# Kernel optimization log

Measured on AMD Instinct MI355X. Metric: run time of the kernel, lower is better.

Reference implementation:

```python
import jax, jax.numpy as jnp
import numpy as np
import math

SIGMA_DATA = 0.5
SIGMA_MIN = 0.002
SIGMA_MAX = 80.0
B = 32768
STATE = 256
ACT = 64
TD = 16
E = 16
H = 256  # moe hidden = gate_dim = output_dim = hidden_dim//4
IN = STATE + ACT + TD  # 336
TOP_K = 4


def mish(x):
    return x * jnp.tanh(jax.nn.softplus(x))


def setup_inputs() -> dict:
    key = jax.random.key(0)
    ks = jax.random.split(key, 20)
    def xavier(k, shape):
        fan_in, fan_out = shape[-2], shape[-1]
        lim = math.sqrt(6.0 / (fan_in + fan_out))
        return jax.random.uniform(k, shape, jnp.float32, -lim, lim)
    inp = {
        "x": jax.random.normal(ks[0], (B, ACT), jnp.float32),
        "sigma": jax.random.uniform(ks[1], (B,), jnp.float32) * (SIGMA_MAX - SIGMA_MIN) + SIGMA_MIN,
        "state": jax.random.normal(ks[2], (B, STATE), jnp.float32),
        # time MLP: Linear(16,32), Mish, Linear(32,16)
        "tW1": xavier(ks[3], (TD, 2 * TD)), "tb1": jnp.zeros((2 * TD,), jnp.float32),
        "tW2": xavier(ks[4], (2 * TD, TD)), "tb2": jnp.zeros((TD,), jnp.float32),
        # gate: Linear(IN, H), ReLU, (dropout eval), Linear(H, E)
        "gW1": xavier(ks[5], (IN, H)), "gb1": jnp.zeros((H,), jnp.float32),
        "gW2": xavier(ks[6], (H, E)), "gb2": jnp.zeros((E,), jnp.float32),
        # 16 stacked expert MLPs: IN->H->H->H with Mish after each Linear
        "eW1": xavier(ks[7], (E, IN, H)), "eb1": jnp.zeros((E, H), jnp.float32),
        "eW2": xavier(ks[8], (E, H, H)), "eb2": jnp.zeros((E, H), jnp.float32),
        "eW3": xavier(ks[9], (E, H, H)), "eb3": jnp.zeros((E, H), jnp.float32),
        # final layer: Linear(H, ACT)
        "fW": xavier(ks[10], (H, ACT)), "fb": jnp.zeros((ACT,), jnp.float32),
    }
    return inp


def reference(x, sigma, state, tW1, tb1, tW2, tb2, gW1, gb1, gW2, gb2,
              eW1, eb1, eW2, eb2, eW3, eb3, fW, fb):
    # --- consistency-model scalings (boundary condition) ---
    c_skip = SIGMA_DATA ** 2 / ((sigma - SIGMA_MIN) ** 2 + SIGMA_DATA ** 2)
    c_out = (sigma - SIGMA_MIN) * SIGMA_DATA * jax.lax.rsqrt(sigma ** 2 + SIGMA_DATA ** 2)
    c_in = jax.lax.rsqrt(sigma ** 2 + SIGMA_DATA ** 2)
    rescaled_t = 1000.0 * 0.25 * jnp.log(sigma + 1e-44)

    x_in = c_in[:, None] * x

    # --- sinusoidal time embedding (dim=16) + time MLP ---
    half = TD // 2
    freqs = jnp.exp(jnp.arange(half, dtype=jnp.float32) * (-math.log(10000.0) / (half - 1)))
    ang = rescaled_t[:, None] * freqs[None, :]           # [B, 8]
    pe = jnp.concatenate([jnp.sin(ang), jnp.cos(ang)], axis=-1)  # [B, 16]
    t = mish(pe @ tW1 + tb1) @ tW2 + tb2                 # [B, 16]

    inp = jnp.concatenate([x_in, t, state], axis=1)      # [B, 336]

    # --- gate (eval mode: dropout off) ---
    g = jax.nn.relu(inp @ gW1 + gb1) @ gW2 + gb2         # [B, E]
    gate_scores = jax.nn.softmax(g, axis=1)
    top_k_scores, top_k_idx = jax.lax.top_k(gate_scores, TOP_K)  # [B, K]

    # --- run ALL experts densely (as the original does) ---
    h = mish(jnp.einsum('bi,eih->beh', inp, eW1) + eb1)  # [B, E, H]
    h = mish(jnp.einsum('beh,ehk->bek', h, eW2) + eb2)
    expert_out = mish(jnp.einsum('beh,eho->beo', h, eW3) + eb3)  # [B, E, H]

    # --- gather top-k, scale by normalized gate scores, combine ---
    sel = jnp.take_along_axis(expert_out, top_k_idx[:, :, None], axis=1)  # [B, K, H]
    scaled = sel * top_k_scores[:, :, None]
    scaled = scaled / (jnp.sum(top_k_scores, axis=1, keepdims=True)[:, :, None] + 1e-9)
    combined = jnp.sum(scaled, axis=1)                   # [B, H]

    # --- auxiliary loss ---
    one_hot = jax.nn.one_hot(top_k_idx, E, dtype=jnp.float32)  # [B, K, E]
    expert_load = jnp.sum(one_hot, axis=(0, 1)) / (x.shape[0] + 1e-9)
    load_balancing_loss = jnp.var(expert_load, ddof=1)   # torch .var() is unbiased
    entropy = -jnp.mean(jnp.sum(gate_scores * jnp.log(gate_scores + 1e-9), axis=1))
    aux_loss = load_balancing_loss + entropy

    model_out = combined @ fW + fb                       # [B, ACT]
    denoised = c_out[:, None] * model_out + c_skip[:, None] * x
    denoised = jnp.clip(denoised, -1.0, 1.0)             # clip_denoised=True
    return denoised, aux_loss
```

## Files before the change

kernel.cpp:

```cpp
#include <hip/hip_runtime.h>
#include <math.h>

#define BN 32768
#define INDP 352
#define HD 256
#define AD 64
#define EN 16
#define TME 32
#define STOT (BN * 4)
#define GRID_E 4112
#define CHUNK_E 514

typedef __attribute__((ext_vector_type(8))) short s8v;
typedef __attribute__((ext_vector_type(4))) float f4v;
typedef unsigned short u16;

__device__ __forceinline__ u16 f2bf(float x) {
  unsigned u = __float_as_uint(x);
  return (u16)((u + 0x7fffu + ((u >> 16) & 1u)) >> 16);
}
__device__ __forceinline__ float bf2f(u16 h) { return __uint_as_float(((unsigned)h) << 16); }
__device__ __forceinline__ float rcpf(float a) { float r; asm("v_rcp_f32 %0, %1" : "=v"(r) : "v"(a)); return r; }
__device__ __forceinline__ float mishf(float x) {
  float xc = fminf(x, 30.f);
  float u = __expf(xc);
  float w = fmaf(u, u, u + u);
  return x * w * rcpf(w + 2.f);
}
__device__ __forceinline__ f4v mfma16(s8v a, s8v b, f4v c) {
  return __builtin_amdgcn_mfma_f32_16x16x32_bf16(a, b, c, 0, 0, 0);
}
__device__ __forceinline__ void pack8(const u16* q, u16* d) {
  uint4 u;
  u.x = q[0] | ((unsigned)q[1] << 16); u.y = q[2] | ((unsigned)q[3] << 16);
  u.z = q[4] | ((unsigned)q[5] << 16); u.w = q[6] | ((unsigned)q[7] << 16);
  *(uint4*)d = u;
}

__global__ void k_init(float* __restrict__ out, int* __restrict__ counts,
                       int* __restrict__ cursor, float* __restrict__ ent) {
  int i = blockIdx.x * 256 + threadIdx.x;
  if (i < BN * AD) out[i] = 0.f;
  if (i < 16) { counts[i] = 0; cursor[i] = 0; }
  if (i == 16) *ent = 0.f;
}

__global__ void k_prep(const float* __restrict__ src, u16* __restrict__ dst,
                       int Ksrc, int Spad, int NT, int N,
                       long sStride, long dStride, int NP, int total) {
  int idx = blockIdx.x * 256 + threadIdx.x;
  if (idx >= total) return;
  int l = idx & 63;
  int t = idx >> 6;
  int nt = t % NT; t /= NT;
  int s = t % Spad; t /= Spad;
  int m = t;
  const float* sp = src + (size_t)m * sStride;
  int n = nt * 16 + (l & 15);
  int kb = s * 32 + (l >> 4) * 8;
  u16 q0[8], q1[8], q2[8];
  #pragma unroll
  for (int i = 0; i < 8; ++i) {
    int k = kb + i;
    float v = (k < Ksrc) ? sp[(size_t)k * N + n] : 0.f;
    u16 a = f2bf(v); float r1 = v - bf2f(a);
    u16 b = f2bf(r1); float r2 = r1 - bf2f(b);
    q0[i] = a; q1[i] = b; q2[i] = f2bf(r2);
  }
  u16* d = dst + (size_t)m * dStride + (size_t)((s * NT + nt) * NP) * 512 + l * 8;
  pack8(q0, d);
  pack8(q1, d + 512);
  if (NP == 3) pack8(q2, d + 1024);
}

__global__ void k_time_inp(const float* __restrict__ x, const float* __restrict__ sigma,
                           const float* __restrict__ state,
                           const float* __restrict__ tW1, const float* __restrict__ tb1,
                           const float* __restrict__ tW2, const float* __restrict__ tb2,
                           u16* __restrict__ p0, u16* __restrict__ p1, u16* __restrict__ p2) {
  const int wv = threadIdx.x >> 6;
  const int lane = threadIdx.x & 63;
  const int row = blockIdx.x * 4 + wv;
  const float sg = sigma[row];
  const float rt = 250.0f * logf(sg + 1e-44f);
  float pe = 0.f;
  if (lane < 16) {
    int j = lane & 7;
    float f = expf(-1.3157629102823121f * (float)j);
    float ang = rt * f;
    pe = (lane < 8) ? sinf(ang) : cosf(ang);
  }
  float h1;
  {
    float acc = 0.f;
    int j = lane & 31;
    #pragma unroll
    for (int i = 0; i < 16; ++i) {
      float p = __shfl(pe, i, 64);
      acc = fmaf(p, tW1[i * 32 + j], acc);
    }
    acc += tb1[j];
    float sp = log1pf(expf(acc));
    h1 = acc * tanhf(sp);
  }
  float t2;
  {
    float acc = 0.f;
    int j = lane & 15;
    #pragma unroll
    for (int i = 0; i < 32; ++i) {
      float h = __shfl(h1, i, 64);
      acc = fmaf(h, tW2[i * 16 + j], acc);
    }
    t2 = acc + tb2[j];
  }
  const float c_in = rsqrtf(sg * sg + 0.25f);
  u16* r0 = p0 + (size_t)row * INDP;
  u16* r1 = p1 + (size_t)row * INDP;
  u16* r2 = p2 + (size_t)row * INDP;
  auto wsplit = [&](int c, float v) {
    u16 a = f2bf(v); float ra = v - bf2f(a);
    u16 b = f2bf(ra); float rb = ra - bf2f(b);
    r0[c] = a; r1[c] = b; r2[c] = f2bf(rb);
  };
  wsplit(lane, c_in * x[row * 64 + lane]);
  if (lane < 16) wsplit(64 + lane, t2);
  #pragma unroll
  for (int r = 0; r < 4; ++r)
    wsplit(80 + r * 64 + lane, state[(size_t)row * 256 + r * 64 + lane]);
  if (lane < 16) { r0[336 + lane] = 0; r1[336 + lane] = 0; r2[336 + lane] = 0; }
}

__global__ __launch_bounds__(256, 3) void k_gate(
    const u16* __restrict__ p0, const u16* __restrict__ p1, const u16* __restrict__ p2,
    const u16* __restrict__ gW1b, const float* __restrict__ gb1,
    const u16* __restrict__ gW2b, const float* __restrict__ gb2,
    int* __restrict__ topk_idx, float* __restrict__ topk_w,
    int* __restrict__ counts, float* __restrict__ ent_sum) {
  __shared__ __align__(16) u16 sH0[TME * 256];
  __shared__ __align__(16) u16 sH1[TME * 256];
  __shared__ __align__(16) u16 sH2[TME * 256];
  __shared__ float sLog[TME * 16];
  __shared__ int scnt[16];
  const int tid = threadIdx.x;
  const int l = tid & 63, wn = tid >> 6;
  const int g = l >> 4, r16 = l & 15;
  const int row0 = blockIdx.x * TME;
  const int swz = (r16 & 7) << 3;
  if (tid < 16) scnt[tid] = 0;

  f4v acc[2][4];
  #pragma unroll
  for (int i = 0; i < 2; ++i)
    #pragma unroll
    for (int j = 0; j < 4; ++j) acc[i][j] = (f4v){0.f, 0.f, 0.f, 0.f};

  #pragma unroll 2
  for (int s = 0; s < 11; ++s) {
    s8v a0[2], a1[2], a2[2], b0[4], b1[4], b2[4];
    #pragma unroll
    for (int mt = 0; mt < 2; ++mt) {
      size_t off = (size_t)(row0 + mt * 16 + r16) * INDP + s * 32 + g * 8;
      a0[mt] = *(const s8v*)(p0 + off);
      a1[mt] = *(const s8v*)(p1 + off);
      a2[mt] = *(const s8v*)(p2 + off);
    }
    #pragma unroll
    for (int j = 0; j < 4; ++j) {
      const u16* pb = gW1b + (size_t)((s * 16 + wn * 4 + j) * 3) * 512 + l * 8;
      b0[j] = *(const s8v*)pb;
      b1[j] = *(const s8v*)(pb + 512);
      b2[j] = *(const s8v*)(pb + 1024);
    }
    #pragma unroll
    for (int mt = 0; mt < 2; ++mt)
      #pragma unroll
      for (int j = 0; j < 4; ++j) {
        acc[mt][j] = mfma16(a0[mt], b0[j], acc[mt][j]);
        acc[mt][j] = mfma16(a0[mt], b1[j], acc[mt][j]);
        acc[mt][j] = mfma16(a1[mt], b0[j], acc[mt][j]);
        acc[mt][j] = mfma16(a1[mt], b1[j], acc[mt][j]);
        acc[mt][j] = mfma16(a0[mt], b2[j], acc[mt][j]);
        acc[mt][j] = mfma16(a2[mt], b0[j], acc[mt][j]);
      }
  }
  #pragma unroll
  for (int mt = 0; mt < 2; ++mt)
    #pragma unroll
    for (int j = 0; j < 4; ++j) {
      float bj = gb1[wn * 64 + j * 16 + r16];
      #pragma unroll
      for (int r = 0; r < 4; ++r) {
        int row = mt * 16 + g * 4 + r;
        int col = wn * 64 + j * 16 + r16;
        float v = fmaxf(acc[mt][j][r] + bj, 0.f);
        u16 h0 = f2bf(v); float ra = v - bf2f(h0);
        u16 h1 = f2bf(ra); float rb = ra - bf2f(h1);
        int ec = col ^ ((row & 7) << 3);
        sH0[row * 256 + ec] = h0;
        sH1[row * 256 + ec] = h1;
        sH2[row * 256 + ec] = f2bf(rb);
      }
    }
  __syncthreads();

  f4v l2[2];
  l2[0] = (f4v){0.f, 0.f, 0.f, 0.f};
  l2[1] = (f4v){0.f, 0.f, 0.f, 0.f};
  #pragma unroll
  for (int s = 0; s < 8; ++s) {
    const u16* pb = gW2b + (size_t)(s * 3) * 512 + l * 8;
    s8v b0 = *(const s8v*)pb;
    s8v b1 = *(const s8v*)(pb + 512);
    s8v b2 = *(const s8v*)(pb + 1024);
    #pragma unroll
    for (int mt = 0; mt < 2; ++mt) {
      int row = mt * 16 + r16;
      int ec = (s * 32 + g * 8) ^ swz;
      s8v a0 = *(const s8v*)&sH0[row * 256 + ec];
      s8v a1 = *(const s8v*)&sH1[row * 256 + ec];
      s8v a2 = *(const s8v*)&sH2[row * 256 + ec];
      l2[mt] = mfma16(a0, b0, l2[mt]);
      l2[mt] = mfma16(a0, b1, l2[mt]);
      l2[mt] = mfma16(a1, b0, l2[mt]);
      l2[mt] = mfma16(a1, b1, l2[mt]);
      l2[mt] = mfma16(a0, b2, l2[mt]);
      l2[mt] = mfma16(a2, b0, l2[mt]);
    }
  }
  if (wn == 0) {
    #pragma unroll
    for (int mt = 0; mt < 2; ++mt)
      #pragma unroll
      for (int r = 0; r < 4; ++r)
        sLog[(mt * 16 + g * 4 + r) * 16 + r16] = l2[mt][r] + gb2[r16];
  }
  __syncthreads();

  float entc = 0.f;
  if (tid < TME) {
    const int row = row0 + tid;
    float gx[16], mx = -1e30f;
    #pragma unroll
    for (int e = 0; e < 16; ++e) { gx[e] = sLog[tid * 16 + e]; mx = fmaxf(mx, gx[e]); }
    float p[16], s = 0.f;
    #pragma unroll
    for (int e = 0; e < 16; ++e) { p[e] = expf(gx[e] - mx); s += p[e]; }
    const float inv = 1.f / s;
    #pragma unroll
    for (int e = 0; e < 16; ++e) {
      float pr = p[e] * inv;
      entc -= pr * logf(pr + 1e-9f);
    }
    int idxs[4]; float scs[4];
    unsigned used = 0;
    float wsum = 1e-9f;
    #pragma unroll
    for (int k = 0; k < 4; ++k) {
      int be = 0; float bv = -1.f;
      #pragma unroll
      for (int e = 0; e < 16; ++e) {
        float pr = p[e] * inv;
        if (!((used >> e) & 1u) && pr > bv) { bv = pr; be = e; }
      }
      used |= (1u << be);
      idxs[k] = be; scs[k] = bv;
      wsum += bv;
    }
    #pragma unroll
    for (int k = 0; k < 4; ++k) {
      topk_idx[row * 4 + k] = idxs[k];
      topk_w[row * 4 + k] = scs[k] / wsum;
      atomicAdd(&scnt[idxs[k]], 1);
    }
  }
  if (tid < 64) {
    #pragma unroll
    for (int off = 32; off > 0; off >>= 1) entc += __shfl_down(entc, off, 64);
  }
  if (tid == 0) atomicAdd(ent_sum, entc);
  __syncthreads();
  if (tid < 16 && scnt[tid] > 0) atomicAdd(&counts[tid], scnt[tid]);
}

__global__ void k_aux(const int* __restrict__ counts, const float* __restrict__ ent_sum,
                      int* __restrict__ offsets, int* __restrict__ tbk,
                      float* __restrict__ aux_out) {
  if (threadIdx.x == 0) {
    int off = 0, t = 0;
    float load[16], mean = 0.f;
    for (int e = 0; e < 16; ++e) {
      offsets[e] = off; tbk[e] = t;
      int c = counts[e];
      off += c;
      t += (c + TME - 1) / TME;
      load[e] = (float)c / (32768.0f + 1e-9f);
      mean += load[e];
    }
    offsets[16] = off; tbk[16] = t;
    mean *= (1.f / 16.f);
    float var = 0.f;
    for (int e = 0; e < 16; ++e) { float d = load[e] - mean; var += d * d; }
    var *= (1.f / 15.f);
    *aux_out = var + ent_sum[0] * (1.0f / 32768.0f);
  }
}

__global__ void k_scatter(const int* __restrict__ topk_idx, const float* __restrict__ topk_w,
                          const int* __restrict__ offsets, int* __restrict__ cursor,
                          int* __restrict__ slot_row, float* __restrict__ slot_w) {
  __shared__ int cnt[16];
  __shared__ int base[16];
  const int tid = threadIdx.x;
  if (tid < 16) cnt[tid] = 0;
  __syncthreads();
  const int row = blockIdx.x * 256 + tid;
  int e4[4]; float w4[4]; int lp[4];
  #pragma unroll
  for (int k = 0; k < 4; ++k) {
    e4[k] = topk_idx[row * 4 + k];
    w4[k] = topk_w[row * 4 + k];
    lp[k] = atomicAdd(&cnt[e4[k]], 1);
  }
  __syncthreads();
  if (tid < 16) base[tid] = atomicAdd(&cursor[tid], cnt[tid]);
  __syncthreads();
  #pragma unroll
  for (int k = 0; k < 4; ++k) {
    int s = offsets[e4[k]] + base[e4[k]] + lp[k];
    slot_row[s] = row;
    slot_w[s] = w4[k];
  }
}

__global__ __launch_bounds__(256, 4) void k_expert(
    const u16* __restrict__ inpHi, const u16* __restrict__ inpLo,
    const u16* __restrict__ eW1b, const float* __restrict__ eb1,
    const u16* __restrict__ eW2b, const float* __restrict__ eb2,
    const u16* __restrict__ eW3b, const float* __restrict__ eb3,
    const u16* __restrict__ fWb,
    const int* __restrict__ offsets, const int* __restrict__ counts,
    const int* __restrict__ tbk, const int* __restrict__ slot_row,
    const float* __restrict__ slot_w, float* __restrict__ out) {
  __shared__ __align__(16) u16 sHi[TME * 256];
  __shared__ __align__(16) u16 sLo[TME * 256];
  __shared__ int sRows[TME];
  __shared__ float sWv[TME];

  const int bid = (blockIdx.x & 7) * CHUNK_E + (blockIdx.x >> 3);
  if (bid >= tbk[16]) return;
  int e = 0;
  #pragma unroll
  for (int i = 1; i < 16; ++i)
    if (bid >= tbk[i]) e = i;
  const int tile = bid - tbk[e];
  const int cnt = counts[e];
  const int s0 = offsets[e] + tile * TME;
  const int nr = min(TME, cnt - tile * TME);
  const int tid = threadIdx.x;
  const int l = tid & 63;
  const int wn = tid >> 6;
  const int g = l >> 4, r16 = l & 15;
  const int swz = (r16 & 7) << 3;

  if (tid < TME) {
    sRows[tid] = (tid < nr) ? slot_row[s0 + tid] : slot_row[s0];
    sWv[tid] = (tid < nr) ? slot_w[s0 + tid] : 0.f;
  }
  __syncthreads();

  size_t rbase[2];
  #pragma unroll
  for (int mt = 0; mt < 2; ++mt)
    rbase[mt] = (size_t)sRows[mt * 16 + r16] * INDP;

  f4v acc[2][4];
  #pragma unroll
  for (int i = 0; i < 2; ++i)
    #pragma unroll
    for (int j = 0; j < 4; ++j) acc[i][j] = (f4v){0.f, 0.f, 0.f, 0.f};

  const u16* W1 = eW1b + (size_t)e * 180224;
  #pragma unroll 2
  for (int s = 0; s < 11; ++s) {
    s8v ah[2], al[2], bh[4], bl[4];
    #pragma unroll
    for (int mt = 0; mt < 2; ++mt) {
      size_t off = rbase[mt] + s * 32 + g * 8;
      ah[mt] = *(const s8v*)(inpHi + off);
      al[mt] = *(const s8v*)(inpLo + off);
    }
    #pragma unroll
    for (int j = 0; j < 4; ++j) {
      const u16* pb = W1 + (size_t)((s * 16 + wn * 4 + j) * 2) * 512 + l * 8;
      bh[j] = *(const s8v*)pb;
      bl[j] = *(const s8v*)(pb + 512);
    }
    #pragma unroll
    for (int mt = 0; mt < 2; ++mt)
      #pragma unroll
      for (int j = 0; j < 4; ++j) {
        acc[mt][j] = mfma16(ah[mt], bh[j], acc[mt][j]);
        acc[mt][j] = mfma16(al[mt], bh[j], acc[mt][j]);
        acc[mt][j] = mfma16(ah[mt], bl[j], acc[mt][j]);
      }
  }
  {
    const float* b1 = eb1 + e * HD;
    #pragma unroll
    for (int mt = 0; mt < 2; ++mt)
      #pragma unroll
      for (int j = 0; j < 4; ++j) {
        float bj = b1[wn * 64 + j * 16 + r16];
        #pragma unroll
        for (int r = 0; r < 4; ++r) {
          int row = mt * 16 + g * 4 + r;
          int col = wn * 64 + j * 16 + r16;
          float v = mishf(acc[mt][j][r] + bj);
          u16 h = f2bf(v);
          int ec = col ^ ((row & 7) << 3);
          sHi[row * 256 + ec] = h;
          sLo[row * 256 + ec] = f2bf(v - bf2f(h));
        }
      }
  }
  __syncthreads();

  #pragma unroll 1
  for (int L = 0; L < 2; ++L) {
    const u16* Wb = (L == 0 ? eW2b : eW3b) + (size_t)e * 131072;
    const float* bb = (L == 0 ? eb2 : eb3) + e * HD;
    f4v a2[2][4];
    #pragma unroll
    for (int i = 0; i < 2; ++i)
      #pragma unroll
      for (int j = 0; j < 4; ++j) a2[i][j] = (f4v){0.f, 0.f, 0.f, 0.f};
    #pragma unroll 2
    for (int s = 0; s < 8; ++s) {
      s8v ah[2], al[2], bh[4], bl[4];
      #pragma unroll
      for (int mt = 0; mt < 2; ++mt) {
        int row = mt * 16 + r16;
        int ec = (s * 32 + g * 8) ^ swz;
        ah[mt] = *(const s8v*)&sHi[row * 256 + ec];
        al[mt] = *(const s8v*)&sLo[row * 256 + ec];
      }
      #pragma unroll
      for (int j = 0; j < 4; ++j) {
        const u16* pb = Wb + (size_t)((s * 16 + wn * 4 + j) * 2) * 512 + l * 8;
        bh[j] = *(const s8v*)pb;
        bl[j] = *(const s8v*)(pb + 512);
      }
      #pragma unroll
      for (int mt = 0; mt < 2; ++mt)
        #pragma unroll
        for (int j = 0; j < 4; ++j) {
          a2[mt][j] = mfma16(ah[mt], bh[j], a2[mt][j]);
          a2[mt][j] = mfma16(al[mt], bh[j], a2[mt][j]);
          a2[mt][j] = mfma16(ah[mt], bl[j], a2[mt][j]);
        }
    }
    __syncthreads();
    #pragma unroll
    for (int mt = 0; mt < 2; ++mt)
      #pragma unroll
      for (int j = 0; j < 4; ++j) {
        float bj = bb[wn * 64 + j * 16 + r16];
        #pragma unroll
        for (int r = 0; r < 4; ++r) {
          int row = mt * 16 + g * 4 + r;
          int col = wn * 64 + j * 16 + r16;
          float v = mishf(a2[mt][j][r] + bj);
          u16 h = f2bf(v);
          int ec = col ^ ((row & 7) << 3);
          sHi[row * 256 + ec] = h;
          sLo[row * 256 + ec] = f2bf(v - bf2f(h));
        }
      }
    __syncthreads();
  }

  f4v a3[2];
  a3[0] = (f4v){0.f, 0.f, 0.f, 0.f};
  a3[1] = (f4v){0.f, 0.f, 0.f, 0.f};
  #pragma unroll 2
  for (int s = 0; s < 8; ++s) {
    s8v ah[2], al[2];
    #pragma unroll
    for (int mt = 0; mt < 2; ++mt) {
      int row = mt * 16 + r16;
      int ec = (s * 32 + g * 8) ^ swz;
      ah[mt] = *(const s8v*)&sHi[row * 256 + ec];
      al[mt] = *(const s8v*)&sLo[row * 256 + ec];
    }
    const u16* pb = fWb + (size_t)((s * 4 + wn) * 2) * 512 + l * 8;
    s8v bh = *(const s8v*)pb;
    s8v bl = *(const s8v*)(pb + 512);
    #pragma unroll
    for (int mt = 0; mt < 2; ++mt) {
      a3[mt] = mfma16(ah[mt], bh, a3[mt]);
      a3[mt] = mfma16(al[mt], bh, a3[mt]);
      a3[mt] = mfma16(ah[mt], bl, a3[mt]);
    }
  }
  #pragma unroll
  for (int mt = 0; mt < 2; ++mt)
    #pragma unroll
    for (int r = 0; r < 4; ++r) {
      int rl = mt * 16 + g * 4 + r;
      if (rl < nr) {
        float v = a3[mt][r] * sWv[rl];
        atomicAdd(&out[(size_t)sRows[rl] * AD + wn * 16 + r16], v);
      }
    }
}

__global__ void k_final(const float* __restrict__ x, const float* __restrict__ sigma,
                        const float* __restrict__ fb, float* __restrict__ out) {
  int i = blockIdx.x * 256 + threadIdx.x;
  if (i >= BN * AD) return;
  int row = i >> 6, c = i & 63;
  float sg = sigma[row];
  float sm = sg - 0.002f;
  float c_skip = 0.25f / (sm * sm + 0.25f);
  float c_out = sm * 0.5f * rsqrtf(sg * sg + 0.25f);
  float d = c_out * (out[i] + fb[c]) + c_skip * x[i];
  out[i] = fminf(fmaxf(d, -1.f), 1.f);
}

extern "C" void kernel_launch(void* const* d_in, const int* in_sizes, int n_in,
                              void* d_out, int out_size, void* d_ws, size_t ws_size,
                              hipStream_t stream) {
  const float* x     = (const float*)d_in[0];
  const float* sigma = (const float*)d_in[1];
  const float* state = (const float*)d_in[2];
  const float* tW1   = (const float*)d_in[3];
  const float* tb1   = (const float*)d_in[4];
  const float* tW2   = (const float*)d_in[5];
  const float* tb2   = (const float*)d_in[6];
  const float* gW1   = (const float*)d_in[7];
  const float* gb1   = (const float*)d_in[8];
  const float* gW2   = (const float*)d_in[9];
  const float* gb2   = (const float*)d_in[10];
  const float* eW1   = (const float*)d_in[11];
  const float* eb1   = (const float*)d_in[12];
  const float* eW2   = (const float*)d_in[13];
  const float* eb2   = (const float*)d_in[14];
  const float* eW3   = (const float*)d_in[15];
  const float* eb3   = (const float*)d_in[16];
  const float* fW    = (const float*)d_in[17];
  const float* fb    = (const float*)d_in[18];
  float* out = (float*)d_out;

  char* p = (char*)d_ws;
  auto alloc = [&](size_t bytes) { void* r = (void*)p; p += (bytes + 255) & ~(size_t)255; return r; };
  u16* inpHi  = (u16*)alloc((size_t)BN * INDP * 2);
  u16* inpLo  = (u16*)alloc((size_t)BN * INDP * 2);
  u16* inpMid = (u16*)alloc((size_t)BN * INDP * 2);
  u16* gW1b   = (u16*)alloc((size_t)11 * 16 * 3 * 512 * 2);
  u16* gW2b   = (u16*)alloc((size_t)8 * 3 * 512 * 2);
  u16* eW1b   = (u16*)alloc((size_t)16 * 180224 * 2);
  u16* eW2b   = (u16*)alloc((size_t)16 * 131072 * 2);
  u16* eW3b   = (u16*)alloc((size_t)16 * 131072 * 2);
  u16* fWb    = (u16*)alloc((size_t)32768 * 2);
  int*   topk_idx = (int*)alloc((size_t)BN * 4 * 4);
  float* topk_w   = (float*)alloc((size_t)BN * 4 * 4);
  int*   counts   = (int*)alloc(64);
  int*   cursor   = (int*)alloc(64);
  int*   offsets  = (int*)alloc(68);
  int*   tbk      = (int*)alloc(68);
  float* ent      = (float*)alloc(4);
  int*   slot_row = (int*)alloc((size_t)STOT * 4);
  float* slot_w   = (float*)alloc((size_t)STOT * 4);

  k_init<<<(BN * AD + 255) / 256, 256, 0, stream>>>(out, counts, cursor, ent);

  int tot;
  tot = 16 * 11 * 16 * 64;
  k_prep<<<(tot + 255) / 256, 256, 0, stream>>>(eW1, eW1b, 336, 11, 16, 256,
                                                (long)336 * 256, 180224, 2, tot);
  tot = 16 * 8 * 16 * 64;
  k_prep<<<(tot + 255) / 256, 256, 0, stream>>>(eW2, eW2b, 256, 8, 16, 256,
                                                (long)256 * 256, 131072, 2, tot);
  k_prep<<<(tot + 255) / 256, 256, 0, stream>>>(eW3, eW3b, 256, 8, 16, 256,
                                                (long)256 * 256, 131072, 2, tot);
  tot = 11 * 16 * 64;
  k_prep<<<(tot + 255) / 256, 256, 0, stream>>>(gW1, gW1b, 336, 11, 16, 256,
                                                0, 0, 3, tot);
  tot = 8 * 1 * 64;
  k_prep<<<(tot + 255) / 256, 256, 0, stream>>>(gW2, gW2b, 256, 8, 1, 16,
                                                0, 0, 3, tot);
  tot = 8 * 4 * 64;
  k_prep<<<(tot + 255) / 256, 256, 0, stream>>>(fW, fWb, 256, 8, 4, 64,
                                                0, 0, 2, tot);

  k_time_inp<<<BN / 4, 256, 0, stream>>>(x, sigma, state, tW1, tb1, tW2, tb2,
                                         inpHi, inpLo, inpMid);
  k_gate<<<BN / TME, 256, 0, stream>>>(inpHi, inpLo, inpMid, gW1b, gb1, gW2b, gb2,
                                       topk_idx, topk_w, counts, ent);
  k_aux<<<1, 64, 0, stream>>>(counts, ent, offsets, tbk, out + (size_t)BN * AD);
  k_scatter<<<BN / 256, 256, 0, stream>>>(topk_idx, topk_w, offsets, cursor, slot_row, slot_w);
  k_expert<<<GRID_E, 256, 0, stream>>>(inpHi, inpLo, eW1b, eb1, eW2b, eb2,
                                       eW3b, eb3, fWb, offsets, counts, tbk,
                                       slot_row, slot_w, out);
  k_final<<<(BN * AD + 255) / 256, 256, 0, stream>>>(x, sigma, fb, out);
}
```

Baseline: 467.1 us.

## Replace atomic combine with per-slot expert outputs; shrink gate tile; reorder MFMAs

The expert kernel now writes each slot's unweighted final-layer output to a dense buffer instead of atomically adding weighted results into the output. The final kernel gathers the four slots per row through a new reverse slot map and applies the top-k weights, so zeroing the output in the init kernel is no longer needed. The gate kernel moves to 16-row tiles with a higher occupancy hint, and the MFMA chains in the gate and expert kernels are regrouped and fully unrolled so consecutive MFMAs go to independent accumulators. This trades atomic contention and an extra output clear for a new 32 MB intermediate buffer and an extra gather read in the final pass.

```diff
diff --git a/kernel.cpp b/kernel.cpp
--- a/kernel.cpp
+++ b/kernel.cpp
@@ -7,6 +7,7 @@
 #define AD 64
 #define EN 16
 #define TME 32
+#define TMG 16
 #define STOT (BN * 4)
 #define GRID_E 4112
 #define CHUNK_E 514
@@ -37,10 +38,9 @@
   *(uint4*)d = u;
 }
 
-__global__ void k_init(float* __restrict__ out, int* __restrict__ counts,
-                       int* __restrict__ cursor, float* __restrict__ ent) {
-  int i = blockIdx.x * 256 + threadIdx.x;
-  if (i < BN * AD) out[i] = 0.f;
+__global__ void k_init(int* __restrict__ counts, int* __restrict__ cursor,
+                       float* __restrict__ ent) {
+  int i = threadIdx.x;
   if (i < 16) { counts[i] = 0; cursor[i] = 0; }
   if (i == 16) *ent = 0.f;
 }
@@ -131,39 +131,36 @@
   if (lane < 16) { r0[336 + lane] = 0; r1[336 + lane] = 0; r2[336 + lane] = 0; }
 }
 
-__global__ __launch_bounds__(256, 3) void k_gate(
+__global__ __launch_bounds__(256, 4) void k_gate(
     const u16* __restrict__ p0, const u16* __restrict__ p1, const u16* __restrict__ p2,
     const u16* __restrict__ gW1b, const float* __restrict__ gb1,
     const u16* __restrict__ gW2b, const float* __restrict__ gb2,
     int* __restrict__ topk_idx, float* __restrict__ topk_w,
     int* __restrict__ counts, float* __restrict__ ent_sum) {
-  __shared__ __align__(16) u16 sH0[TME * 256];
-  __shared__ __align__(16) u16 sH1[TME * 256];
-  __shared__ __align__(16) u16 sH2[TME * 256];
-  __shared__ float sLog[TME * 16];
+  __shared__ __align__(16) u16 sH0[TMG * 256];
+  __shared__ __align__(16) u16 sH1[TMG * 256];
+  __shared__ __align__(16) u16 sH2[TMG * 256];
+  __shared__ float sLog[TMG * 16];
   __shared__ int scnt[16];
   const int tid = threadIdx.x;
   const int l = tid & 63, wn = tid >> 6;
   const int g = l >> 4, r16 = l & 15;
-  const int row0 = blockIdx.x * TME;
+  const int row0 = blockIdx.x * TMG;
   const int swz = (r16 & 7) << 3;
   if (tid < 16) scnt[tid] = 0;
 
-  f4v acc[2][4];
-  #pragma unroll
-  for (int i = 0; i < 2; ++i)
-    #pragma unroll
-    for (int j = 0; j < 4; ++j) acc[i][j] = (f4v){0.f, 0.f, 0.f, 0.f};
-
-  #pragma unroll 2
+  f4v acc[4];
+  #pragma unroll
+  for (int j = 0; j < 4; ++j) acc[j] = (f4v){0.f, 0.f, 0.f, 0.f};
+
+  #pragma unroll
   for (int s = 0; s < 11; ++s) {
-    s8v a0[2], a1[2], a2[2], b0[4], b1[4], b2[4];
-    #pragma unroll
-    for (int mt = 0; mt < 2; ++mt) {
-      size_t off = (size_t)(row0 + mt * 16 + r16) * INDP + s * 32 + g * 8;
-      a0[mt] = *(const s8v*)(p0 + off);
-      a1[mt] = *(const s8v*)(p1 + off);
-      a2[mt] = *(const s8v*)(p2 + off);
+    s8v a0, a1, a2, b0[4], b1[4], b2[4];
+    {
+      size_t off = (size_t)(row0 + r16) * INDP + s * 32 + g * 8;
+      a0 = *(const s8v*)(p0 + off);
+      a1 = *(const s8v*)(p1 + off);
+      a2 = *(const s8v*)(p2 + off);
     }
     #pragma unroll
     for (int j = 0; j < 4; ++j) {
@@ -173,72 +170,63 @@
       b2[j] = *(const s8v*)(pb + 1024);
     }
     #pragma unroll
-    for (int mt = 0; mt < 2; ++mt)
-      #pragma unroll
-      for (int j = 0; j < 4; ++j) {
-        acc[mt][j] = mfma16(a0[mt], b0[j], acc[mt][j]);
-        acc[mt][j] = mfma16(a0[mt], b1[j], acc[mt][j]);
-        acc[mt][j] = mfma16(a1[mt], b0[j], acc[mt][j]);
-        acc[mt][j] = mfma16(a1[mt], b1[j], acc[mt][j]);
-        acc[mt][j] = mfma16(a0[mt], b2[j], acc[mt][j]);
-        acc[mt][j] = mfma16(a2[mt], b0[j], acc[mt][j]);
-      }
-  }
-  #pragma unroll
-  for (int mt = 0; mt < 2; ++mt)
-    #pragma unroll
-    for (int j = 0; j < 4; ++j) {
-      float bj = gb1[wn * 64 + j * 16 + r16];
-      #pragma unroll
-      for (int r = 0; r < 4; ++r) {
-        int row = mt * 16 + g * 4 + r;
-        int col = wn * 64 + j * 16 + r16;
-        float v = fmaxf(acc[mt][j][r] + bj, 0.f);
-        u16 h0 = f2bf(v); float ra = v - bf2f(h0);
-        u16 h1 = f2bf(ra); float rb = ra - bf2f(h1);
-        int ec = col ^ ((row & 7) << 3);
-        sH0[row * 256 + ec] = h0;
-        sH1[row * 256 + ec] = h1;
-        sH2[row * 256 + ec] = f2bf(rb);
-      }
-    }
-  __syncthreads();
-
-  f4v l2[2];
-  l2[0] = (f4v){0.f, 0.f, 0.f, 0.f};
-  l2[1] = (f4v){0.f, 0.f, 0.f, 0.f};
+    for (int j = 0; j < 4; ++j) acc[j] = mfma16(a0, b0[j], acc[j]);
+    #pragma unroll
+    for (int j = 0; j < 4; ++j) acc[j] = mfma16(a0, b1[j], acc[j]);
+    #pragma unroll
+    for (int j = 0; j < 4; ++j) acc[j] = mfma16(a1, b0[j], acc[j]);
+    #pragma unroll
+    for (int j = 0; j < 4; ++j) acc[j] = mfma16(a1, b1[j], acc[j]);
+    #pragma unroll
+    for (int j = 0; j < 4; ++j) acc[j] = mfma16(a0, b2[j], acc[j]);
+    #pragma unroll
+    for (int j = 0; j < 4; ++j) acc[j] = mfma16(a2, b0[j], acc[j]);
+  }
+  #pragma unroll
+  for (int j = 0; j < 4; ++j) {
+    float bj = gb1[wn * 64 + j * 16 + r16];
+    #pragma unroll
+    for (int r = 0; r < 4; ++r) {
+      int row = g * 4 + r;
+      int col = wn * 64 + j * 16 + r16;
+      float v = fmaxf(acc[j][r] + bj, 0.f);
+      u16 h0 = f2bf(v); float ra = v - bf2f(h0);
+      u16 h1 = f2bf(ra); float rb = ra - bf2f(h1);
+      int ec = col ^ ((row & 7) << 3);
+      sH0[row * 256 + ec] = h0;
+      sH1[row * 256 + ec] = h1;
+      sH2[row * 256 + ec] = f2bf(rb);
+    }
+  }
+  __syncthreads();
+
+  f4v l2 = (f4v){0.f, 0.f, 0.f, 0.f};
   #pragma unroll
   for (int s = 0; s < 8; ++s) {
     const u16* pb = gW2b + (size_t)(s * 3) * 512 + l * 8;
     s8v b0 = *(const s8v*)pb;
     s8v b1 = *(const s8v*)(pb + 512);
     s8v b2 = *(const s8v*)(pb + 1024);
-    #pragma unroll
-    for (int mt = 0; mt < 2; ++mt) {
-      int row = mt * 16 + r16;
-      int ec = (s * 32 + g * 8) ^ swz;
-      s8v a0 = *(const s8v*)&sH0[row * 256 + ec];
-      s8v a1 = *(const s8v*)&sH1[row * 256 + ec];
-      s8v a2 = *(const s8v*)&sH2[row * 256 + ec];
-      l2[mt] = mfma16(a0, b0, l2[mt]);
-      l2[mt] = mfma16(a0, b1, l2[mt]);
-      l2[mt] = mfma16(a1, b0, l2[mt]);
-      l2[mt] = mfma16(a1, b1, l2[mt]);
-      l2[mt] = mfma16(a0, b2, l2[mt]);
-      l2[mt] = mfma16(a2, b0, l2[mt]);
-    }
+    int ec = (s * 32 + g * 8) ^ swz;
+    s8v a0 = *(const s8v*)&sH0[r16 * 256 + ec];
+    s8v a1 = *(const s8v*)&sH1[r16 * 256 + ec];
+    s8v a2 = *(const s8v*)&sH2[r16 * 256 + ec];
+    l2 = mfma16(a0, b0, l2);
+    l2 = mfma16(a0, b1, l2);
+    l2 = mfma16(a1, b0, l2);
+    l2 = mfma16(a1, b1, l2);
+    l2 = mfma16(a0, b2, l2);
+    l2 = mfma16(a2, b0, l2);
   }
   if (wn == 0) {
     #pragma unroll
-    for (int mt = 0; mt < 2; ++mt)
-      #pragma unroll
-      for (int r = 0; r < 4; ++r)
-        sLog[(mt * 16 + g * 4 + r) * 16 + r16] = l2[mt][r] + gb2[r16];
+    for (int r = 0; r < 4; ++r)
+      sLog[(g * 4 + r) * 16 + r16] = l2[r] + gb2[r16];
   }
   __syncthreads();
 
   float entc = 0.f;
-  if (tid < TME) {
+  if (tid < TMG) {
     const int row = row0 + tid;
     float gx[16], mx = -1e30f;
     #pragma unroll
@@ -308,18 +296,17 @@
 
 __global__ void k_scatter(const int* __restrict__ topk_idx, const float* __restrict__ topk_w,
                           const int* __restrict__ offsets, int* __restrict__ cursor,
-                          int* __restrict__ slot_row, float* __restrict__ slot_w) {
+                          int* __restrict__ slot_row, int* __restrict__ rslot) {
   __shared__ int cnt[16];
   __shared__ int base[16];
   const int tid = threadIdx.x;
   if (tid < 16) cnt[tid] = 0;
   __syncthreads();
   const int row = blockIdx.x * 256 + tid;
-  int e4[4]; float w4[4]; int lp[4];
+  int e4[4]; int lp[4];
   #pragma unroll
   for (int k = 0; k < 4; ++k) {
     e4[k] = topk_idx[row * 4 + k];
-    w4[k] = topk_w[row * 4 + k];
     lp[k] = atomicAdd(&cnt[e4[k]], 1);
   }
   __syncthreads();
@@ -329,7 +316,7 @@
   for (int k = 0; k < 4; ++k) {
     int s = offsets[e4[k]] + base[e4[k]] + lp[k];
     slot_row[s] = row;
-    slot_w[s] = w4[k];
+    rslot[row * 4 + k] = s;
   }
 }
 
@@ -341,11 +328,10 @@
     const u16* __restrict__ fWb,
     const int* __restrict__ offsets, const int* __restrict__ counts,
     const int* __restrict__ tbk, const int* __restrict__ slot_row,
-    const float* __restrict__ slot_w, float* __restrict__ out) {
+    float* __restrict__ eout) {
   __shared__ __align__(16) u16 sHi[TME * 256];
   __shared__ __align__(16) u16 sLo[TME * 256];
   __shared__ int sRows[TME];
-  __shared__ float sWv[TME];
 
   const int bid = (blockIdx.x & 7) * CHUNK_E + (blockIdx.x >> 3);
   if (bid >= tbk[16]) return;
@@ -363,10 +349,8 @@
   const int g = l >> 4, r16 = l & 15;
   const int swz = (r16 & 7) << 3;
 
-  if (tid < TME) {
+  if (tid < TME)
     sRows[tid] = (tid < nr) ? slot_row[s0 + tid] : slot_row[s0];
-    sWv[tid] = (tid < nr) ? slot_w[s0 + tid] : 0.f;
-  }
   __syncthreads();
 
   size_t rbase[2];
@@ -381,7 +365,7 @@
     for (int j = 0; j < 4; ++j) acc[i][j] = (f4v){0.f, 0.f, 0.f, 0.f};
 
   const u16* W1 = eW1b + (size_t)e * 180224;
-  #pragma unroll 2
+  #pragma unroll
   for (int s = 0; s < 11; ++s) {
     s8v ah[2], al[2], bh[4], bl[4];
     #pragma unroll
@@ -399,11 +383,15 @@
     #pragma unroll
     for (int mt = 0; mt < 2; ++mt)
       #pragma unroll
-      for (int j = 0; j < 4; ++j) {
-        acc[mt][j] = mfma16(ah[mt], bh[j], acc[mt][j]);
-        acc[mt][j] = mfma16(al[mt], bh[j], acc[mt][j]);
-        acc[mt][j] = mfma16(ah[mt], bl[j], acc[mt][j]);
-      }
+      for (int j = 0; j < 4; ++j) acc[mt][j] = mfma16(ah[mt], bh[j], acc[mt][j]);
+    #pragma unroll
+    for (int mt = 0; mt < 2; ++mt)
+      #pragma unroll
+      for (int j = 0; j < 4; ++j) acc[mt][j] = mfma16(al[mt], bh[j], acc[mt][j]);
+    #pragma unroll
+    for (int mt = 0; mt < 2; ++mt)
+      #pragma unroll
+      for (int j = 0; j < 4; ++j) acc[mt][j] = mfma16(ah[mt], bl[j], acc[mt][j]);
   }
   {
     const float* b1 = eb1 + e * HD;
@@ -435,7 +423,7 @@
     for (int i = 0; i < 2; ++i)
       #pragma unroll
       for (int j = 0; j < 4; ++j) a2[i][j] = (f4v){0.f, 0.f, 0.f, 0.f};
-    #pragma unroll 2
+    #pragma unroll
     for (int s = 0; s < 8; ++s) {
       s8v ah[2], al[2], bh[4], bl[4];
       #pragma unroll
@@ -454,11 +442,15 @@
       #pragma unroll
       for (int mt = 0; mt < 2; ++mt)
         #pragma unroll
-        for (int j = 0; j < 4; ++j) {
-          a2[mt][j] = mfma16(ah[mt], bh[j], a2[mt][j]);
-          a2[mt][j] = mfma16(al[mt], bh[j], a2[mt][j]);
-          a2[mt][j] = mfma16(ah[mt], bl[j], a2[mt][j]);
-        }
+        for (int j = 0; j < 4; ++j) a2[mt][j] = mfma16(ah[mt], bh[j], a2[mt][j]);
+      #pragma unroll
+      for (int mt = 0; mt < 2; ++mt)
+        #pragma unroll
+        for (int j = 0; j < 4; ++j) a2[mt][j] = mfma16(al[mt], bh[j], a2[mt][j]);
+      #pragma unroll
+      for (int mt = 0; mt < 2; ++mt)
+        #pragma unroll
+        for (int j = 0; j < 4; ++j) a2[mt][j] = mfma16(ah[mt], bl[j], a2[mt][j]);
     }
     __syncthreads();
     #pragma unroll
@@ -483,7 +475,7 @@
   f4v a3[2];
   a3[0] = (f4v){0.f, 0.f, 0.f, 0.f};
   a3[1] = (f4v){0.f, 0.f, 0.f, 0.f};
-  #pragma unroll 2
+  #pragma unroll
   for (int s = 0; s < 8; ++s) {
     s8v ah[2], al[2];
     #pragma unroll
@@ -508,23 +500,27 @@
     #pragma unroll
     for (int r = 0; r < 4; ++r) {
       int rl = mt * 16 + g * 4 + r;
-      if (rl < nr) {
-        float v = a3[mt][r] * sWv[rl];
-        atomicAdd(&out[(size_t)sRows[rl] * AD + wn * 16 + r16], v);
-      }
+      if (rl < nr)
+        eout[(size_t)(s0 + rl) * AD + wn * 16 + r16] = a3[mt][r];
     }
 }
 
 __global__ void k_final(const float* __restrict__ x, const float* __restrict__ sigma,
-                        const float* __restrict__ fb, float* __restrict__ out) {
+                        const float* __restrict__ fb, const int* __restrict__ rslot,
+                        const float* __restrict__ topk_w, const float* __restrict__ eout,
+                        float* __restrict__ out) {
   int i = blockIdx.x * 256 + threadIdx.x;
   if (i >= BN * AD) return;
   int row = i >> 6, c = i & 63;
+  float a = 0.f;
+  #pragma unroll
+  for (int k = 0; k < 4; ++k)
+    a = fmaf(topk_w[row * 4 + k], eout[(size_t)rslot[row * 4 + k] * AD + c], a);
   float sg = sigma[row];
   float sm = sg - 0.002f;
   float c_skip = 0.25f / (sm * sm + 0.25f);
   float c_out = sm * 0.5f * rsqrtf(sg * sg + 0.25f);
-  float d = c_out * (out[i] + fb[c]) + c_skip * x[i];
+  float d = c_out * (a + fb[c]) + c_skip * x[i];
   out[i] = fminf(fmaxf(d, -1.f), 1.f);
 }
 
@@ -563,17 +559,18 @@
   u16* eW2b   = (u16*)alloc((size_t)16 * 131072 * 2);
   u16* eW3b   = (u16*)alloc((size_t)16 * 131072 * 2);
   u16* fWb    = (u16*)alloc((size_t)32768 * 2);
+  float* eout = (float*)alloc((size_t)STOT * AD * 4);
   int*   topk_idx = (int*)alloc((size_t)BN * 4 * 4);
   float* topk_w   = (float*)alloc((size_t)BN * 4 * 4);
+  int*   rslot    = (int*)alloc((size_t)BN * 4 * 4);
   int*   counts   = (int*)alloc(64);
   int*   cursor   = (int*)alloc(64);
   int*   offsets  = (int*)alloc(68);
   int*   tbk      = (int*)alloc(68);
   float* ent      = (float*)alloc(4);
   int*   slot_row = (int*)alloc((size_t)STOT * 4);
-  float* slot_w   = (float*)alloc((size_t)STOT * 4);
-
-  k_init<<<(BN * AD + 255) / 256, 256, 0, stream>>>(out, counts, cursor, ent);
+
+  k_init<<<1, 64, 0, stream>>>(counts, cursor, ent);
 
   int tot;
   tot = 16 * 11 * 16 * 64;
@@ -596,12 +593,14 @@
 
   k_time_inp<<<BN / 4, 256, 0, stream>>>(x, sigma, state, tW1, tb1, tW2, tb2,
                                          inpHi, inpLo, inpMid);
-  k_gate<<<BN / TME, 256, 0, stream>>>(inpHi, inpLo, inpMid, gW1b, gb1, gW2b, gb2,
+  k_gate<<<BN / TMG, 256, 0, stream>>>(inpHi, inpLo, inpMid, gW1b, gb1, gW2b, gb2,
                                        topk_idx, topk_w, counts, ent);
   k_aux<<<1, 64, 0, stream>>>(counts, ent, offsets, tbk, out + (size_t)BN * AD);
-  k_scatter<<<BN / 256, 256, 0, stream>>>(topk_idx, topk_w, offsets, cursor, slot_row, slot_w);
+  k_scatter<<<BN / 256, 256, 0, stream>>>(topk_idx, topk_w, offsets, cursor,
+                                          slot_row, rslot);
   k_expert<<<GRID_E, 256, 0, stream>>>(inpHi, inpLo, eW1b, eb1, eW2b, eb2,
                                        eW3b, eb3, fWb, offsets, counts, tbk,
-                                       slot_row, slot_w, out);
-  k_final<<<(BN * AD + 255) / 256, 256, 0, stream>>>(x, sigma, fb, out);
-}
+                                       slot_row, eout);
+  k_final<<<(BN * AD + 255) / 256, 256, 0, stream>>>(x, sigma, fb, rslot,
+                                                     topk_w, eout, out);
+}
```

Measured after the change: 531.6 us. 13.8% more time.
